# Kernel tuning notes

Measured on AMD Instinct MI355X. Metric: run time of the kernel, lower is better.

The kernel has to match this reference:

```python
import jax, jax.numpy as jnp
import numpy as np

B, D = 256, 2048
DT = 0.1           # RK4 step size (init arg dt)
MAX_DELTA_T = 5.0  # from get_stop_condition(max_delta_t=5.0)
TOL = 0.01         # from get_stop_condition(tolerance=0.01)
N_STEPS = int(MAX_DELTA_T / DT)  # 50 RK4 steps max
EPS = 1e-8         # epsilon in the custom sqrt gradient


def setup_inputs() -> dict:
    key = jax.random.key(0)
    k1, k2 = jax.random.split(key)
    x0 = jax.random.normal(k1, (B, D), dtype=jnp.float32)
    W = jax.random.normal(k2, (D, D), dtype=jnp.float32) * (1.0 / np.float32(np.sqrt(D)))
    b = jnp.zeros((D,), dtype=jnp.float32)
    return {"x0": x0, "W": W, "b": b}


def _pvf(x, W, b):
    # Energy E(x) = 5 * sqrt(sum(tanh(x@W + b)^2, axis=1))  (per-sample, summed for grad)
    # pvf = -dE/dx, using the module's custom sqrt gradient 0.5*dy/(y + 1e-8):
    #   dE/dh = 5 * h / (y + eps);  dh/dz = 1 - h^2;  dz/dx = W^T
    h = jnp.tanh(x @ W + b)                 # [B, D]
    y = jnp.sqrt(jnp.sum(h * h, axis=1))    # [B]
    coef = 5.0 / (y + EPS)                  # [B]
    grad_x = (coef[:, None] * h * (1.0 - h * h)) @ W.T  # [B, D]
    return -grad_x


def reference(x0, W, b):
    # Hopfield gradient flow dx/dt = pvf(x), integrated with RK4.
    # Dynamic stop (max|pvf| < tol) realized as a freeze mask inside a fixed-length scan.
    def step(carry, _):
        x, done = carry
        k1 = _pvf(x, W, b)
        done = jnp.logical_or(done, jnp.max(jnp.abs(k1)) < TOL)
        k2 = _pvf(x + 0.5 * DT * k1, W, b)
        k3 = _pvf(x + 0.5 * DT * k2, W, b)
        k4 = _pvf(x + DT * k3, W, b)
        x_new = x + (DT / 6.0) * (k1 + 2.0 * k2 + 2.0 * k3 + k4)
        x = jnp.where(done, x, x_new)
        return (x, done), None

    (y, _), _ = jax.lax.scan(step, (x0, jnp.array(False)), None, length=N_STEPS)
    return y
```

## Files before the change

### kernel.cpp

```cpp
#include <hip/hip_runtime.h>
#include <math.h>

#define BDIM 256
#define DDIM 2048
constexpr float DT    = 0.1f;
constexpr float TOL   = 0.01f;
constexpr int   NSTEP = 50;
constexpr float EPS_  = 1e-8f;

typedef __attribute__((ext_vector_type(8))) short short8;
typedef __attribute__((ext_vector_type(4))) float f32x4;

__device__ __forceinline__ ushort f2bf(float f) {
    unsigned u = __float_as_uint(f);
    return (ushort)((u + 0x7fffu + ((u >> 16) & 1u)) >> 16);
}
__device__ __forceinline__ float bf2f(ushort h) { return __uint_as_float(((unsigned)h) << 16); }

#define GLOAD_LDS16(g, l) __builtin_amdgcn_global_load_lds( \
    (const __attribute__((address_space(1))) void*)(g),      \
    (__attribute__((address_space(3))) void*)(l), 16, 0, 0)

#define MFMA16(a, b, c) __builtin_amdgcn_mfma_f32_16x16x32_bf16((a), (b), (c), 0, 0, 0)

template<int NT>
__device__ __forceinline__ f32x4 gemm_core(ushort* lds,
    const ushort* __restrict__ Ahg, const ushort* __restrict__ Alg,
    const ushort* __restrict__ Bhg, const ushort* __restrict__ Blg,
    int row0, int col0)
{
    constexpr int NSP    = (NT == 3) ? 4 : (NT == 2) ? 3 : 2;
    constexpr int KS     = (NT == 1) ? 256 : 128;
    constexpr int ITERS  = 2048 / KS;
    constexpr int SPSZ   = 32 * KS;
    constexpr int STRIDE = NSP * SPSZ;
    constexpr int BOFF   = (NT >= 2) ? 2 * SPSZ : SPSZ;
    constexpr int NJ     = SPSZ / 512;

    const int t = threadIdx.x, lane = t & 63, wid = t >> 6;
    const int wr = wid >> 1, wc = wid & 1;
    const int fr = lane & 15, cq = lane >> 4;

    const ushort* sp_src = (wid == 0) ? Ahg : (wid == 1) ? Alg : (wid == 2) ? Bhg : Blg;
    const int sp_base = (wid < 2) ? row0 : col0;
    const int slot = (NT == 1 && wid == 2) ? 1 : wid;
    const bool do_stage = (NT == 3) || (NT == 2 && wid < 3)
                       || (NT == 1 && (wid == 0 || wid == 2));

    auto stage = [&](int it, int db) {
        if (!do_stage) return;
        ushort* L = lds + db * STRIDE + slot * SPSZ;
        #pragma unroll
        for (int j = 0; j < NJ; ++j) {
            int r, c;
            if constexpr (NT == 1) { r = 2 * j + (lane >> 5); c = lane & 31; }
            else                   { r = 4 * j + (lane >> 4); c = lane & 15; }
            const ushort* g = sp_src + (size_t)(sp_base + r) * DDIM + it * KS
                              + ((c ^ (r & 7)) * 8);
            GLOAD_LDS16(g, L + j * 512 + lane * 8);
        }
    };

    f32x4 acc_e = {0.f, 0.f, 0.f, 0.f};
    f32x4 acc_o = {0.f, 0.f, 0.f, 0.f};

    const int arow = wr * 16 + fr, brow = wc * 16 + fr;
    const int aoffb = arow * KS, boffb = brow * KS;
    const int sa = arow & 7, sb = brow & 7;

    stage(0, 0);
    __syncthreads();

    for (int it = 0; it < ITERS; ++it) {
        const int db = it & 1;
        if (it < ITERS - 1) stage(it + 1, db ^ 1);
        const ushort* L = lds + db * STRIDE;
        #pragma unroll
        for (int ks = 0; ks < KS / 32; ++ks) {
            const int ca = ((ks * 4 + cq) ^ sa) * 8;
            const int cb = ((ks * 4 + cq) ^ sb) * 8;
            const short8 ah = *(const short8*)&L[       aoffb + ca];
            const short8 bh = *(const short8*)&L[BOFF + boffb + cb];
            f32x4& acc = (ks & 1) ? acc_o : acc_e;
            acc = MFMA16(ah, bh, acc);
            if constexpr (NT >= 2) {
                const short8 al = *(const short8*)&L[SPSZ + aoffb + ca];
                acc = MFMA16(al, bh, acc);
            }
            if constexpr (NT == 3) {
                const short8 bl = *(const short8*)&L[3 * SPSZ + boffb + cb];
                acc = MFMA16(ah, bl, acc);
            }
        }
        __syncthreads();
    }

    f32x4 acc;
    #pragma unroll
    for (int j = 0; j < 4; ++j) acc[j] = acc_e[j] + acc_o[j];
    return acc;
}

__global__ __launch_bounds__(256)
void prep_w_k(const float* __restrict__ W, ushort* __restrict__ Wh, ushort* __restrict__ Wl)
{
    const size_t i = ((size_t)blockIdx.x * 256 + threadIdx.x) * 4;
    const float4 v = *(const float4*)(W + i);
    ushort4 h, l;
    h.x = f2bf(v.x); l.x = f2bf(v.x - bf2f(h.x));
    h.y = f2bf(v.y); l.y = f2bf(v.y - bf2f(h.y));
    h.z = f2bf(v.z); l.z = f2bf(v.z - bf2f(h.z));
    h.w = f2bf(v.w); l.w = f2bf(v.w - bf2f(h.w));
    *(ushort4*)(Wh + i) = h;
    *(ushort4*)(Wl + i) = l;
}

__global__ __launch_bounds__(256)
void prep_wt_k(const float* __restrict__ W, ushort* __restrict__ Wth, ushort* __restrict__ Wtl)
{
    __shared__ float T[64][65];
    const int t = threadIdx.x;
    const int k0 = blockIdx.y * 64, n0 = blockIdx.x * 64;
    const int r = t >> 2, c4 = (t & 3) * 16;
    const float* src = W + (size_t)(k0 + r) * DDIM + n0 + c4;
    #pragma unroll
    for (int j = 0; j < 4; ++j) {
        const float4 v = *(const float4*)(src + j * 4);
        T[r][c4 + j*4 + 0] = v.x; T[r][c4 + j*4 + 1] = v.y;
        T[r][c4 + j*4 + 2] = v.z; T[r][c4 + j*4 + 3] = v.w;
    }
    __syncthreads();
    ushort hb[16], lb[16];
    #pragma unroll
    for (int j = 0; j < 16; ++j) {
        const float v = T[c4 + j][r];
        hb[j] = f2bf(v); lb[j] = f2bf(v - bf2f(hb[j]));
    }
    ushort* oh = Wth + (size_t)(n0 + r) * DDIM + k0 + c4;
    ushort* ol = Wtl + (size_t)(n0 + r) * DDIM + k0 + c4;
    #pragma unroll
    for (int q = 0; q < 4; ++q) {
        *(ushort4*)(oh + q*4) = make_ushort4(hb[q*4], hb[q*4+1], hb[q*4+2], hb[q*4+3]);
        *(ushort4*)(ol + q*4) = make_ushort4(lb[q*4], lb[q*4+1], lb[q*4+2], lb[q*4+3]);
    }
}

__global__ __launch_bounds__(256)
void init10_k(const float* __restrict__ x0,
              ushort* __restrict__ Bh, ushort* __restrict__ Bl,
              float* __restrict__ Utot, float* __restrict__ csum,
              unsigned* __restrict__ maxu, int* __restrict__ done)
{
    const size_t i = ((size_t)blockIdx.x * 256 + threadIdx.x) * 4;
    const float4 v = *(const float4*)(x0 + i);
    ushort4 h, l;
    h.x = f2bf(v.x); l.x = f2bf(v.x - bf2f(h.x));
    h.y = f2bf(v.y); l.y = f2bf(v.y - bf2f(h.y));
    h.z = f2bf(v.z); l.z = f2bf(v.z - bf2f(h.z));
    h.w = f2bf(v.w); l.w = f2bf(v.w - bf2f(h.w));
    *(ushort4*)(Bh + i) = h;
    *(ushort4*)(Bl + i) = l;
    *(float4*)(Utot + i) = make_float4(0.f, 0.f, 0.f, 0.f);
    if (blockIdx.x == 0) {
        for (int j = threadIdx.x; j < 1024; j += 256) csum[j] = 0.f;
        if (threadIdx.x == 0) { *maxu = 0u; *done = 0; }
    }
}

__global__ __launch_bounds__(256, 2)
void gbuild_mm(const ushort* __restrict__ Wth, const ushort* __restrict__ Wtl,
               ushort* __restrict__ Gh, ushort* __restrict__ Gl)
{
    __shared__ __align__(16) ushort lds[32768];
    const int id = blockIdx.x;
    const int bx = id & 63, by = id >> 6;
    const f32x4 acc = gemm_core<3>(lds, Wth, Wtl, Wth, Wtl, by * 32, bx * 32);

    const int lane = threadIdx.x & 63, wid = threadIdx.x >> 6;
    const int r0 = by * 32 + (wid >> 1) * 16 + (lane >> 4) * 4;
    const int c0 = bx * 32 + (wid & 1) * 16 + (lane & 15);
    #pragma unroll
    for (int j = 0; j < 4; ++j) {
        const size_t idx = (size_t)(r0 + j) * DDIM + c0;
        const ushort gh = f2bf(acc[j]);
        Gh[idx] = gh; Gl[idx] = f2bf(acc[j] - bf2f(gh));
    }
}

template<int MODE>
__global__ __launch_bounds__(256, 2)
void hop10_mm(const ushort* __restrict__ Ahg, const ushort* __restrict__ Alg,
              const ushort* __restrict__ Bhg, const ushort* __restrict__ Blg,
              const float* __restrict__ bias,
              float* __restrict__ z, float* __restrict__ S, float* __restrict__ Utot,
              const float* __restrict__ cs_cf, const float* __restrict__ cs_acc,
              float* __restrict__ cs_out, float* __restrict__ cs_zero,
              ushort* oPh, ushort* oPl,
              float w_acc, float cstage,
              const float* __restrict__ x0, float* __restrict__ outb,
              unsigned* __restrict__ maxu, int* __restrict__ done)
{
    constexpr int ZM = (MODE == 7) ? 1 : (MODE == 8) ? 2 : MODE;

    if constexpr (MODE == 8) {
        if (blockIdx.x == 0 && threadIdx.x == 0) {
            if (!*done && __uint_as_float(*maxu) < TOL) *done = 1;
            *maxu = 0u;
        }
    }
    if constexpr (MODE != 0 && MODE != 6) {
        if (*done) return;
    }

    constexpr int NT = (MODE == 6) ? 3 : (MODE == 0) ? 2 : 1;
    constexpr int LDSZ = (NT == 3) ? 32768 : (NT == 2) ? 24576 : 32768;
    __shared__ __align__(16) ushort lds[LDSZ];

    if constexpr (MODE == 7) {
        if (blockIdx.x & 1) {
            const int sid = blockIdx.x >> 1;
            const int sbx = (sid & 7) * 8 + ((sid >> 3) & 7);
            const int sby = sid >> 6;
            const f32x4 sacc = gemm_core<1>(lds, Ahg, nullptr, Blg, nullptr,
                                            sby * 32, sbx * 32);
            const int lane = threadIdx.x & 63, swid = threadIdx.x >> 6;
            const int sr0 = sby * 32 + (swid >> 1) * 16 + (lane >> 4) * 4;
            float mx = 0.f;
            #pragma unroll
            for (int j = 0; j < 4; ++j) {
                const float cf = 5.0f / (sqrtf(cs_cf[sr0 + j]) + EPS_);
                mx = fmaxf(mx, cf * fabsf(sacc[j]));
            }
            #pragma unroll
            for (int m = 1; m <= 32; m <<= 1) mx = fmaxf(mx, __shfl_xor(mx, m));
            if (lane == 0) atomicMax(maxu, __float_as_uint(mx));
            return;
        }
    }

    const int id  = (MODE == 7) ? (blockIdx.x >> 1) : blockIdx.x;
    const int bx  = (id & 7) * 8 + ((id >> 3) & 7);
    const int by  = id >> 6;

    const f32x4 acc = gemm_core<NT>(lds, Ahg, Alg, Bhg,
                                    (NT == 3) ? Blg : nullptr, by * 32, bx * 32);

    const int t = threadIdx.x, lane = t & 63, wid = t >> 6;
    const int fr = lane & 15;
    const int r0 = by * 32 + (wid >> 1) * 16 + (lane >> 4) * 4;
    const int c0 = bx * 32 + (wid & 1) * 16 + fr;

    if constexpr (MODE == 6) {
        #pragma unroll
        for (int j = 0; j < 4; ++j) {
            const size_t idx = (size_t)(r0 + j) * DDIM + c0;
            outb[idx] = x0[idx] - acc[j];
        }
        return;
    }

    float s2[4];
    #pragma unroll
    for (int j = 0; j < 4; ++j) {
        const int row = r0 + j;
        const size_t idx = (size_t)row * DDIM + c0;
        float zs;
        if constexpr (ZM == 0) {
            zs = acc[j] + bias[c0];
            z[idx] = zs;
        } else {
            const float cf = 5.0f / (sqrtf(cs_cf[row]) + EPS_);
            const float kz = -cf * acc[j];
            if constexpr (ZM == 1) { S[idx] = kz; zs = z[idx] + cstage * kz; }
            if constexpr (ZM == 2) { S[idx] += 2.f * kz; zs = z[idx] + cstage * kz; }
            if constexpr (ZM == 4) { zs = z[idx] + (DT / 6.0f) * (S[idx] + kz); z[idx] = zs; }
            if (w_acc != 0.f) {
                const float ua  = bf2f(oPh[idx]) + bf2f(oPl[idx]);
                const float cfa = 5.0f / (sqrtf(cs_acc[row]) + EPS_);
                Utot[idx] += w_acc * cfa * ua;
            }
        }
        const float h = tanhf(zs);
        s2[j] = h * h;
        const float u = h * (1.f - h * h);
        const ushort uh = f2bf(u);
        oPh[idx] = uh; oPl[idx] = f2bf(u - bf2f(uh));
    }
    #pragma unroll
    for (int m = 1; m <= 8; m <<= 1)
        #pragma unroll
        for (int j = 0; j < 4; ++j) s2[j] += __shfl_xor(s2[j], m);
    if (fr == 0) {
        #pragma unroll
        for (int j = 0; j < 4; ++j) atomicAdd(&cs_out[r0 + j], s2[j]);
    }

    if (cs_zero && blockIdx.x == 0) cs_zero[t] = 0.f;
}

__global__ __launch_bounds__(256)
void tailsplit_k(float* __restrict__ Utot, const float* __restrict__ cs4,
                 ushort* bh, ushort* bl, const int* __restrict__ done)
{
    const size_t base = ((size_t)blockIdx.x * 256 + threadIdx.x) * 4;
    const int row = (int)(base >> 11);
    const int add = !(*done);
    float4 u = *(const float4*)(Utot + base);
    if (add) {
        const float cfa = (DT / 6.0f) * 5.0f / (sqrtf(cs4[row]) + EPS_);
        const ushort4 ph = *(const ushort4*)(bh + base);
        const ushort4 pl = *(const ushort4*)(bl + base);
        u.x += cfa * (bf2f(ph.x) + bf2f(pl.x));
        u.y += cfa * (bf2f(ph.y) + bf2f(pl.y));
        u.z += cfa * (bf2f(ph.z) + bf2f(pl.z));
        u.w += cfa * (bf2f(ph.w) + bf2f(pl.w));
    }
    ushort4 h, l;
    h.x = f2bf(u.x); l.x = f2bf(u.x - bf2f(h.x));
    h.y = f2bf(u.y); l.y = f2bf(u.y - bf2f(h.y));
    h.z = f2bf(u.z); l.z = f2bf(u.z - bf2f(h.z));
    h.w = f2bf(u.w); l.w = f2bf(u.w - bf2f(h.w));
    *(ushort4*)(bh + base) = h;
    *(ushort4*)(bl + base) = l;
}

extern "C" void kernel_launch(void* const* d_in, const int* in_sizes, int n_in,
                              void* d_out, int out_size, void* d_ws, size_t ws_size,
                              hipStream_t stream)
{
    const float* x0   = (const float*)d_in[0];
    const float* W    = (const float*)d_in[1];
    const float* bias = (const float*)d_in[2];
    float* out = (float*)d_out;

    const size_t NE = (size_t)BDIM * DDIM;
    const size_t M4 = (size_t)DDIM * DDIM;

    float* ws = (float*)d_ws;
    float* z    = ws;
    float* S    = ws + NE;
    float* Utot = ws + 2 * NE;
    float* csum = ws + 3 * NE;
    unsigned* maxu = (unsigned*)(csum + 1024);
    int*      done = (int*)(maxu + 1);
    ushort* us = (ushort*)(ws + 3 * NE + 1032);
    ushort* bAh = us;
    ushort* bAl = us + NE;
    ushort* bBh = us + 2 * NE;
    ushort* bBl = us + 3 * NE;
    ushort* Gh  = us + 4 * NE;
    ushort* Gl  = Gh + M4;
    ushort* Wxh = Gl + M4;
    ushort* Wxl = Wxh + M4;

    float* cs1 = csum, *cs2 = csum + 256, *cs3 = csum + 512, *cs4 = csum + 768;
    constexpr float W16 = DT / 6.0f, W13 = DT / 3.0f;

    prep_wt_k<<<dim3(32, 32), 256, 0, stream>>>(W, Wxh, Wxl);
    init10_k <<<512, 256, 0, stream>>>(x0, bBh, bBl, Utot, csum, maxu, done);
    hop10_mm<0><<<512, 256, 0, stream>>>(bBh, bBl, Wxh, Wxl, bias,
                                         z, S, Utot, nullptr, nullptr, cs1, nullptr,
                                         bAh, bAl, 0.f, 0.f, nullptr, nullptr, maxu, done);
    gbuild_mm<<<4096, 256, 0, stream>>>(Wxh, Wxl, Gh, Gl);
    prep_w_k <<<4096, 256, 0, stream>>>(W, Wxh, Wxl);

    for (int s = 0; s < NSTEP; ++s) {
        hop10_mm<7><<<1024, 256, 0, stream>>>(bAh, bAl, Gh, Wxh, nullptr,
                                              z, S, Utot, cs1, cs4, cs2, cs3,
                                              bBh, bBl, (s == 0) ? 0.f : W16, 0.5f * DT,
                                              nullptr, nullptr, maxu, done);
        hop10_mm<8><<<512, 256, 0, stream>>>(bBh, bBl, Gh, nullptr, nullptr,
                                             z, S, Utot, cs2, cs1, cs3, cs4,
                                             bAh, bAl, W16, 0.5f * DT,
                                             nullptr, nullptr, maxu, done);
        hop10_mm<2><<<512, 256, 0, stream>>>(bAh, bAl, Gh, nullptr, nullptr,
                                             z, S, Utot, cs3, cs2, cs4, cs1,
                                             bBh, bBl, W13, DT,
                                             nullptr, nullptr, maxu, done);
        hop10_mm<4><<<512, 256, 0, stream>>>(bBh, bBl, Gh, nullptr, nullptr,
                                             z, S, Utot, cs4, cs3, cs1, cs2,
                                             bAh, bAl, W13, 0.f,
                                             nullptr, nullptr, maxu, done);
    }

    tailsplit_k<<<512, 256, 0, stream>>>(Utot, cs4, bBh, bBl, done);
    hop10_mm<6><<<512, 256, 0, stream>>>(bBh, bBl, Wxh, Wxl, nullptr,
                                         z, S, Utot, nullptr, nullptr, nullptr, nullptr,
                                         nullptr, nullptr, 0.f, 0.f,
                                         x0, out, maxu, done);
}
```

Before: 6.004 ms.

## Split-K single-term GEMM across two wave teams with LDS reduction

The single-precision-term GEMM path (NT==1) now runs with 512 threads per block. Two teams of four waves each handle half of the K dimension, using 128-wide K slices with their own double-buffered LDS, and the partial accumulators are summed through LDS at the end. The per-step RK4 kernels (modes 7, 8, 2, 4) are launched with 512 threads and return early from the extra team after the reduction. The aim is to shorten the serial K loop and raise waves per CU to hide latency. The cost is an extra barrier and LDS reduction, plus idle threads during the epilogue.

```diff
diff --git a/kernel.cpp b/kernel.cpp
--- a/kernel.cpp
+++ b/kernel.cpp
@@ -29,76 +29,128 @@
     const ushort* __restrict__ Bhg, const ushort* __restrict__ Blg,
     int row0, int col0)
 {
-    constexpr int NSP    = (NT == 3) ? 4 : (NT == 2) ? 3 : 2;
-    constexpr int KS     = (NT == 1) ? 256 : 128;
-    constexpr int ITERS  = 2048 / KS;
-    constexpr int SPSZ   = 32 * KS;
-    constexpr int STRIDE = NSP * SPSZ;
-    constexpr int BOFF   = (NT >= 2) ? 2 * SPSZ : SPSZ;
-    constexpr int NJ     = SPSZ / 512;
-
-    const int t = threadIdx.x, lane = t & 63, wid = t >> 6;
-    const int wr = wid >> 1, wc = wid & 1;
-    const int fr = lane & 15, cq = lane >> 4;
-
-    const ushort* sp_src = (wid == 0) ? Ahg : (wid == 1) ? Alg : (wid == 2) ? Bhg : Blg;
-    const int sp_base = (wid < 2) ? row0 : col0;
-    const int slot = (NT == 1 && wid == 2) ? 1 : wid;
-    const bool do_stage = (NT == 3) || (NT == 2 && wid < 3)
-                       || (NT == 1 && (wid == 0 || wid == 2));
-
-    auto stage = [&](int it, int db) {
-        if (!do_stage) return;
-        ushort* L = lds + db * STRIDE + slot * SPSZ;
+    if constexpr (NT == 1) {
+        const int t = threadIdx.x, lane = t & 63, wid = t >> 6;
+        const int team = wid >> 2, twid = wid & 3;
+        const int wr = twid >> 1, wc = twid & 1;
+        const int fr = lane & 15, cq = lane >> 4;
+        const int koff = team * 1024;
+
+        const ushort* sp_src = (twid < 2) ? Ahg : Bhg;
+        const int sp_base = (twid < 2) ? row0 : col0;
+        const int slot = (twid >= 2) ? 1 : 0;
+        const bool do_stage = (twid == 0 || twid == 2);
+        ushort* Lbase = lds + team * 16384;
+
+        auto stage = [&](int it, int db) {
+            if (!do_stage) return;
+            ushort* L = Lbase + db * 8192 + slot * 4096;
+            #pragma unroll
+            for (int j = 0; j < 8; ++j) {
+                const int r = 4 * j + (lane >> 4);
+                const ushort* g = sp_src + (size_t)(sp_base + r) * DDIM + koff
+                                  + it * 128 + (((lane & 15) ^ (r & 7)) * 8);
+                GLOAD_LDS16(g, L + j * 512 + lane * 8);
+            }
+        };
+
+        f32x4 acc_e = {0.f, 0.f, 0.f, 0.f};
+        f32x4 acc_o = {0.f, 0.f, 0.f, 0.f};
+        const int arow = wr * 16 + fr, brow = wc * 16 + fr;
+        const int aoffb = arow * 128, boffb = brow * 128;
+        const int sa = arow & 7, sb = brow & 7;
+
+        stage(0, 0);
+        __syncthreads();
+        for (int it = 0; it < 8; ++it) {
+            const int db = it & 1;
+            if (it < 7) stage(it + 1, db ^ 1);
+            const ushort* L = Lbase + db * 8192;
+            #pragma unroll
+            for (int ks = 0; ks < 4; ++ks) {
+                const int ca = ((ks * 4 + cq) ^ sa) * 8;
+                const int cb = ((ks * 4 + cq) ^ sb) * 8;
+                const short8 ah = *(const short8*)&L[       aoffb + ca];
+                const short8 bh = *(const short8*)&L[4096 + boffb + cb];
+                f32x4& acc = (ks & 1) ? acc_o : acc_e;
+                acc = MFMA16(ah, bh, acc);
+            }
+            __syncthreads();
+        }
+
+        f32x4 acc;
         #pragma unroll
-        for (int j = 0; j < NJ; ++j) {
-            int r, c;
-            if constexpr (NT == 1) { r = 2 * j + (lane >> 5); c = lane & 31; }
-            else                   { r = 4 * j + (lane >> 4); c = lane & 15; }
-            const ushort* g = sp_src + (size_t)(sp_base + r) * DDIM + it * KS
-                              + ((c ^ (r & 7)) * 8);
-            GLOAD_LDS16(g, L + j * 512 + lane * 8);
-        }
-    };
-
-    f32x4 acc_e = {0.f, 0.f, 0.f, 0.f};
-    f32x4 acc_o = {0.f, 0.f, 0.f, 0.f};
-
-    const int arow = wr * 16 + fr, brow = wc * 16 + fr;
-    const int aoffb = arow * KS, boffb = brow * KS;
-    const int sa = arow & 7, sb = brow & 7;
-
-    stage(0, 0);
-    __syncthreads();
-
-    for (int it = 0; it < ITERS; ++it) {
-        const int db = it & 1;
-        if (it < ITERS - 1) stage(it + 1, db ^ 1);
-        const ushort* L = lds + db * STRIDE;
+        for (int j = 0; j < 4; ++j) acc[j] = acc_e[j] + acc_o[j];
+
+        float* red = (float*)lds;
+        if (team == 1) *(f32x4*)&red[(t - 256) * 4] = acc;
+        __syncthreads();
+        if (team == 0) acc += *(const f32x4*)&red[t * 4];
+        return acc;
+    } else {
+        constexpr int NSP    = (NT == 3) ? 4 : 3;
+        constexpr int SPSZ   = 4096;
+        constexpr int STRIDE = NSP * SPSZ;
+        constexpr int BOFF   = 2 * SPSZ;
+
+        const int t = threadIdx.x, lane = t & 63, wid = t >> 6;
+        const int wr = wid >> 1, wc = wid & 1;
+        const int fr = lane & 15, cq = lane >> 4;
+
+        const ushort* sp_src = (wid == 0) ? Ahg : (wid == 1) ? Alg
+                             : (wid == 2) ? Bhg : Blg;
+        const int sp_base = (wid < 2) ? row0 : col0;
+        const bool do_stage = (NT == 3) || (wid < 3);
+
+        auto stage = [&](int it, int db) {
+            if (!do_stage) return;
+            ushort* L = lds + db * STRIDE + wid * SPSZ;
+            #pragma unroll
+            for (int j = 0; j < 8; ++j) {
+                const int r = 4 * j + (lane >> 4);
+                const ushort* g = sp_src + (size_t)(sp_base + r) * DDIM
+                                  + it * 128 + (((lane & 15) ^ (r & 7)) * 8);
+                GLOAD_LDS16(g, L + j * 512 + lane * 8);
+            }
+        };
+
+        f32x4 acc_e = {0.f, 0.f, 0.f, 0.f};
+        f32x4 acc_o = {0.f, 0.f, 0.f, 0.f};
+        const int arow = wr * 16 + fr, brow = wc * 16 + fr;
+        const int aoffb = arow * 128, boffb = brow * 128;
+        const int sa = arow & 7, sb = brow & 7;
+
+        stage(0, 0);
+        __syncthreads();
+        for (int it = 0; it < 16; ++it) {
+            const int db = it & 1;
+            if (it < 15) stage(it + 1, db ^ 1);
+            const ushort* L = lds + db * STRIDE;
+            #pragma unroll
+            for (int ks = 0; ks < 4; ++ks) {
+                const int ca = ((ks * 4 + cq) ^ sa) * 8;
+                const int cb = ((ks * 4 + cq) ^ sb) * 8;
+                const short8 ah = *(const short8*)&L[       aoffb + ca];
+                const short8 bh = *(const short8*)&L[BOFF + boffb + cb];
+                f32x4& acc = (ks & 1) ? acc_o : acc_e;
+                acc = MFMA16(ah, bh, acc);
+                {
+                    const short8 al = *(const short8*)&L[SPSZ + aoffb + ca];
+                    acc = MFMA16(al, bh, acc);
+                }
+                if constexpr (NT == 3) {
+                    const short8 bl = *(const short8*)&L[3 * SPSZ + boffb + cb];
+                    acc = MFMA16(ah, bl, acc);
+                }
+            }
+            __syncthreads();
+        }
+
+        f32x4 acc;
         #pragma unroll
-        for (int ks = 0; ks < KS / 32; ++ks) {
-            const int ca = ((ks * 4 + cq) ^ sa) * 8;
-            const int cb = ((ks * 4 + cq) ^ sb) * 8;
-            const short8 ah = *(const short8*)&L[       aoffb + ca];
-            const short8 bh = *(const short8*)&L[BOFF + boffb + cb];
-            f32x4& acc = (ks & 1) ? acc_o : acc_e;
-            acc = MFMA16(ah, bh, acc);
-            if constexpr (NT >= 2) {
-                const short8 al = *(const short8*)&L[SPSZ + aoffb + ca];
-                acc = MFMA16(al, bh, acc);
-            }
-            if constexpr (NT == 3) {
-                const short8 bl = *(const short8*)&L[3 * SPSZ + boffb + cb];
-                acc = MFMA16(ah, bl, acc);
-            }
-        }
-        __syncthreads();
-    }
-
-    f32x4 acc;
-    #pragma unroll
-    for (int j = 0; j < 4; ++j) acc[j] = acc_e[j] + acc_o[j];
-    return acc;
+        for (int j = 0; j < 4; ++j) acc[j] = acc_e[j] + acc_o[j];
+        return acc;
+    }
 }
 
 __global__ __launch_bounds__(256)
@@ -188,7 +240,8 @@
 }
 
 template<int MODE>
-__global__ __launch_bounds__(256, 2)
+__global__ __launch_bounds__((MODE == 0 || MODE == 6) ? 256 : 512,
+                             (MODE == 0 || MODE == 6) ? 2 : 4)
 void hop10_mm(const ushort* __restrict__ Ahg, const ushort* __restrict__ Alg,
               const ushort* __restrict__ Bhg, const ushort* __restrict__ Blg,
               const float* __restrict__ bias,
@@ -223,6 +276,7 @@
             const int sby = sid >> 6;
             const f32x4 sacc = gemm_core<1>(lds, Ahg, nullptr, Blg, nullptr,
                                             sby * 32, sbx * 32);
+            if (threadIdx.x >= 256) return;
             const int lane = threadIdx.x & 63, swid = threadIdx.x >> 6;
             const int sr0 = sby * 32 + (swid >> 1) * 16 + (lane >> 4) * 4;
             float mx = 0.f;
@@ -244,6 +298,9 @@
 
     const f32x4 acc = gemm_core<NT>(lds, Ahg, Alg, Bhg,
                                     (NT == 3) ? Blg : nullptr, by * 32, bx * 32);
+    if constexpr (NT == 1) {
+        if (threadIdx.x >= 256) return;
+    }
 
     const int t = threadIdx.x, lane = t & 63, wid = t >> 6;
     const int fr = lane & 15;
@@ -365,19 +422,19 @@
     prep_w_k <<<4096, 256, 0, stream>>>(W, Wxh, Wxl);
 
     for (int s = 0; s < NSTEP; ++s) {
-        hop10_mm<7><<<1024, 256, 0, stream>>>(bAh, bAl, Gh, Wxh, nullptr,
+        hop10_mm<7><<<1024, 512, 0, stream>>>(bAh, bAl, Gh, Wxh, nullptr,
                                               z, S, Utot, cs1, cs4, cs2, cs3,
                                               bBh, bBl, (s == 0) ? 0.f : W16, 0.5f * DT,
                                               nullptr, nullptr, maxu, done);
-        hop10_mm<8><<<512, 256, 0, stream>>>(bBh, bBl, Gh, nullptr, nullptr,
+        hop10_mm<8><<<512, 512, 0, stream>>>(bBh, bBl, Gh, nullptr, nullptr,
                                              z, S, Utot, cs2, cs1, cs3, cs4,
                                              bAh, bAl, W16, 0.5f * DT,
                                              nullptr, nullptr, maxu, done);
-        hop10_mm<2><<<512, 256, 0, stream>>>(bAh, bAl, Gh, nullptr, nullptr,
+        hop10_mm<2><<<512, 512, 0, stream>>>(bAh, bAl, Gh, nullptr, nullptr,
                                              z, S, Utot, cs3, cs2, cs4, cs1,
                                              bBh, bBl, W13, DT,
                                              nullptr, nullptr, maxu, done);
-        hop10_mm<4><<<512, 256, 0, stream>>>(bBh, bBl, Gh, nullptr, nullptr,
+        hop10_mm<4><<<512, 512, 0, stream>>>(bBh, bBl, Gh, nullptr, nullptr,
                                              z, S, Utot, cs4, cs3, cs1, cs2,
                                              bAh, bAl, W13, 0.f,
                                              nullptr, nullptr, maxu, done);
```

Measured after the change: 6.252 ms. 4.1% more time.
